# Kernel tuning notes

Hardware: AMD Instinct MI355X
Metric: run time of the kernel (lower is better)

The kernel has to match this reference:

```python
import jax, jax.numpy as jnp
import numpy as np

K = 3  # kernel size
PAD = 1
STRIDE = 1


def conv3x3(x, w, b):
    # x: [B,C,H,W], w: [O,I,3,3], b: [O]
    y = jax.lax.conv_general_dilated(
        x, w, window_strides=(STRIDE, STRIDE), padding=[(PAD, PAD), (PAD, PAD)],
        dimension_numbers=("NCHW", "OIHW", "NCHW"))
    return y + b[None, :, None, None]


def deform_conv2d(x, offsets, w, b):
    # x: [B,C,H,W]; offsets: [B,2*K*K,H,W] layout (dy,dx) per kernel tap;
    # w: [O,C,K,K]; b: [O]. stride=1, pad=1, dilation=1 (matches module).
    B, C, H, W = x.shape
    K2 = K * K
    off = offsets.reshape(B, K2, 2, H, W)
    dy, dx = off[:, :, 0], off[:, :, 1]  # [B,K2,H,W]

    ki, kj = jnp.meshgrid(jnp.arange(K), jnp.arange(K), indexing="ij")
    rel_y = (ki - PAD).reshape(K2).astype(x.dtype)  # kernel tap offsets
    rel_x = (kj - PAD).reshape(K2).astype(x.dtype)
    hh = jnp.arange(H, dtype=x.dtype)
    ww = jnp.arange(W, dtype=x.dtype)

    # sampling positions [B,K2,H,W]
    py = hh[None, None, :, None] + rel_y[None, :, None, None] + dy
    px = ww[None, None, None, :] + rel_x[None, :, None, None] + dx

    y0 = jnp.floor(py)
    x0 = jnp.floor(px)
    wy = py - y0  # bilinear weights
    wx = px - x0
    y0i = y0.astype(jnp.int32)
    x0i = x0.astype(jnp.int32)

    xf = x.reshape(B, C, H * W)

    def gather(yi, xi):
        valid = ((yi >= 0) & (yi < H) & (xi >= 0) & (xi < W)).astype(x.dtype)
        yc = jnp.clip(yi, 0, H - 1)
        xc = jnp.clip(xi, 0, W - 1)
        idx = (yc * W + xc).reshape(B, 1, K2 * H * W)
        v = jnp.take_along_axis(xf, idx, axis=2).reshape(B, C, K2, H, W)
        return v * valid.reshape(B, 1, K2, H, W)

    w00 = ((1 - wy) * (1 - wx))[:, None]  # [B,1,K2,H,W]
    w01 = ((1 - wy) * wx)[:, None]
    w10 = (wy * (1 - wx))[:, None]
    w11 = (wy * wx)[:, None]

    val = (w00 * gather(y0i, x0i) + w01 * gather(y0i, x0i + 1)
           + w10 * gather(y0i + 1, x0i) + w11 * gather(y0i + 1, x0i + 1))
    # accumulate over channels and kernel taps
    out = jnp.einsum("ock,bckhw->bohw", w.reshape(w.shape[0], C, K2), val)
    return out + b[None, :, None, None]


def setup_inputs() -> dict:
    key = jax.random.key(0)
    k1, k2, k3, k4 = jax.random.split(key, 4)
    B, Cin, Cout, H, W = 4, 256, 256, 80, 80
    x = jax.random.normal(k1, (B, Cin, H, W), dtype=jnp.float32)
    # offset-predicting conv: small init so predicted offsets are modest
    offset_w = jax.random.normal(k2, (2 * K * K, Cin, 3, 3), dtype=jnp.float32) * 0.01
    offset_b = jnp.zeros((2 * K * K,), dtype=jnp.float32)
    conv_w = jax.random.normal(k3, (Cout, Cin, K, K), dtype=jnp.float32) * (1.0 / np.sqrt(Cin * K * K))
    conv_b = jax.random.normal(k4, (Cout,), dtype=jnp.float32) * 0.01
    return {"x": x, "offset_w": offset_w, "offset_b": offset_b,
            "conv_w": conv_w, "conv_b": conv_b}


def reference(x, offset_w, offset_b, conv_w, conv_b):
    offsets = conv3x3(x, offset_w, offset_b)
    return deform_conv2d(x, offsets, conv_w, conv_b)
```

## Files before the change

### kernel.cpp

```cpp
#include <hip/hip_runtime.h>

#define CB 4
#define CIN 256
#define COUT 256
#define HH 80
#define WW 80
#define HW (HH*WW)
#define K2 9
#define NKC 72
#define LDSROW 56
#define NSTRIP (HW/64)
#define NBLK (CB*NSTRIP)

typedef unsigned short ushort_t;
typedef __attribute__((ext_vector_type(8))) short bf16x8;
typedef __attribute__((ext_vector_type(4))) float f32x4;

__device__ __forceinline__ ushort_t f2bf(float f) {
    unsigned int b = __float_as_uint(f);
    b += 0x7fffu + ((b >> 16) & 1u);
    return (ushort_t)(b >> 16);
}
__device__ __forceinline__ float bflo(unsigned int u) { return __uint_as_float(u << 16); }
__device__ __forceinline__ float bfhi(unsigned int u) { return __uint_as_float(u & 0xffff0000u); }

__device__ __forceinline__ unsigned int blendpack(unsigned int a, unsigned int b,
                                                  unsigned int c, unsigned int d,
                                                  float w0, float w1, float w2, float w3) {
    float lo = w0*bflo(a) + w1*bflo(b) + w2*bflo(c) + w3*bflo(d);
    float hi = w0*bfhi(a) + w1*bfhi(b) + w2*bfhi(c) + w3*bfhi(d);
    unsigned int r;
    asm("v_cvt_pk_bf16_f32 %0, %1, %2" : "=v"(r) : "v"(lo), "v"(hi));
    return r;
}

__global__ __launch_bounds__(256) void prep(const float* __restrict__ x,
                                            const float* __restrict__ conv_w,
                                            const float* __restrict__ offset_w,
                                            ushort_t* __restrict__ xb,
                                            ushort_t* __restrict__ wmain,
                                            ushort_t* __restrict__ woff) {
    __shared__ ushort_t tile[64*256];
    const int tid = threadIdx.x;
    if (blockIdx.x < NBLK) {
        const int b = blockIdx.x / NSTRIP;
        const int hw0 = (blockIdx.x % NSTRIP) * 64;
        const int px4 = (tid & 15) * 4;
        const int cb0 = tid >> 4;
        const float* xp = x + (size_t)b*CIN*HW + hw0 + px4;
        #pragma unroll
        for (int p = 0; p < 16; ++p) {
            const int c = cb0 * 16 + p;
            const float4 v = *(const float4*)(xp + (size_t)c*HW);
            const int blk = c >> 3, sub = c & 7;
            tile[(px4+0)*256 + (((blk) ^ ((px4+0)&31))<<3) + sub] = f2bf(v.x);
            tile[(px4+1)*256 + (((blk) ^ ((px4+1)&31))<<3) + sub] = f2bf(v.y);
            tile[(px4+2)*256 + (((blk) ^ ((px4+2)&31))<<3) + sub] = f2bf(v.z);
            tile[(px4+3)*256 + (((blk) ^ ((px4+3)&31))<<3) + sub] = f2bf(v.w);
        }
        __syncthreads();
        const int g = tid & 31;
        #pragma unroll
        for (int p = 0; p < 8; ++p) {
            const int px = (tid >> 5) + p*8;
            const uint4 r = *(const uint4*)&tile[px*256 + ((g ^ (px&31))<<3)];
            *(uint4*)&xb[((size_t)b*HW + hw0 + px)*CIN + g*8] = r;
        }
    } else {
        const int t = (blockIdx.x - NBLK) * 256 + tid;
        if (t < NKC*16*64) {
            const int kc = t >> 10;
            const int mt = (t >> 6) & 15;
            const int l  = t & 63;
            const int m  = mt*16 + (l & 15);
            const int kb = kc*32 + ((l >> 4) << 3);
            ushort_t v[8];
            #pragma unroll
            for (int i = 0; i < 8; ++i) {
                const int kg = kb + i;
                const int tap = kg >> 8;
                const int c = kg & 255;
                v[i] = f2bf(conv_w[(size_t)(m*CIN + c)*K2 + tap]);
            }
            uint4 r;
            r.x = v[0] | ((unsigned)v[1] << 16);
            r.y = v[2] | ((unsigned)v[3] << 16);
            r.z = v[4] | ((unsigned)v[5] << 16);
            r.w = v[6] | ((unsigned)v[7] << 16);
            *(uint4*)&wmain[(size_t)t*8] = r;
        } else if (t < NKC*16*64 + NKC*2*64) {
            const int t2 = t - NKC*16*64;
            const int kc = t2 >> 7;
            const int mt = (t2 >> 6) & 1;
            const int l  = t2 & 63;
            const int m  = mt*16 + (l & 15);
            const int kb = kc*32 + ((l >> 4) << 3);
            ushort_t v[8];
            #pragma unroll
            for (int i = 0; i < 8; ++i) {
                const int kg = kb + i;
                const int tap = kg >> 8;
                const int c = kg & 255;
                v[i] = (m < 18) ? f2bf(offset_w[(size_t)(m*CIN + c)*K2 + tap]) : (ushort_t)0;
            }
            uint4 r;
            r.x = v[0] | ((unsigned)v[1] << 16);
            r.y = v[2] | ((unsigned)v[3] << 16);
            r.z = v[4] | ((unsigned)v[5] << 16);
            r.w = v[6] | ((unsigned)v[7] << 16);
            *(uint4*)&woff[(size_t)t2*8] = r;
        }
    }
}

template<int BUF>
__device__ __forceinline__ void p3step(int kc, const ushort_t* __restrict__ xbase,
                                       const ushort_t* __restrict__ wmain,
                                       ushort_t* __restrict__ ldsB,
                                       const float (&bw)[K2][64][4], const int (&bi)[K2][64][4],
                                       uint4 &A0, uint4 &A1, uint4 &A2, uint4 &A3, float4 &wtA,
                                       bf16x8 (&afU)[4], bf16x8 (&afI)[4], f32x4 (&acc)[4][4],
                                       int pxg, int cg, int lane, int mt0) {
    float4 wtT; int4 ixT;
    const bool have = (kc + 2) < NKC;
    if (have) {
        const int tapT = (kc + 2) >> 3;
        wtT = *(const float4*)bw[tapT][pxg];
        ixT = *(const int4*)bi[tapT][pxg];
    }
    if (kc + 1 < NKC) {
        #pragma unroll
        for (int mi = 0; mi < 4; ++mi)
            afI[mi] = *(const bf16x8*)(wmain + ((size_t)((kc+1)*16 + mt0 + mi)*64 + lane)*8);
    }
    uint4 r;
    r.x = blendpack(A0.x, A1.x, A2.x, A3.x, wtA.x, wtA.y, wtA.z, wtA.w);
    r.y = blendpack(A0.y, A1.y, A2.y, A3.y, wtA.x, wtA.y, wtA.z, wtA.w);
    r.z = blendpack(A0.z, A1.z, A2.z, A3.z, wtA.x, wtA.y, wtA.z, wtA.w);
    r.w = blendpack(A0.w, A1.w, A2.w, A3.w, wtA.x, wtA.y, wtA.z, wtA.w);
    *(uint4*)&ldsB[BUF*64*LDSROW + pxg*LDSROW + cg*8] = r;
    if (have) {
        const int c0n = ((kc+2) & 7)*32 + cg*8;
        A0 = *(const uint4*)(xbase + ixT.x + c0n);
        A1 = *(const uint4*)(xbase + ixT.y + c0n);
        A2 = *(const uint4*)(xbase + ixT.z + c0n);
        A3 = *(const uint4*)(xbase + ixT.w + c0n);
        wtA = wtT;
    }
    asm volatile("s_waitcnt lgkmcnt(0)" ::: "memory");
    __builtin_amdgcn_s_barrier();
    bf16x8 bfr[4];
    #pragma unroll
    for (int ni = 0; ni < 4; ++ni)
        bfr[ni] = *(const bf16x8*)&ldsB[BUF*64*LDSROW + (ni*16 + (lane&15))*LDSROW + (lane>>4)*8];
    #pragma unroll
    for (int mi = 0; mi < 4; ++mi)
        #pragma unroll
        for (int ni = 0; ni < 4; ++ni)
            acc[mi][ni] = __builtin_amdgcn_mfma_f32_16x16x32_bf16(afU[mi], bfr[ni], acc[mi][ni], 0, 0, 0);
}

__global__ __launch_bounds__(256) void deform_main(const ushort_t* __restrict__ xb,
                                                   const ushort_t* __restrict__ wmain,
                                                   const ushort_t* __restrict__ woff,
                                                   const float* __restrict__ offset_b,
                                                   const float* __restrict__ conv_b,
                                                   float* __restrict__ out) {
    __shared__ __align__(16) char lds_pool[20480];
    __shared__ float off_lds[18][64];
    __shared__ float bw[K2][64][4];
    __shared__ int   bi[K2][64][4];

    const int tid = threadIdx.x;
    const int lane = tid & 63;
    const int wv = tid >> 6;
    const int sb = (blockIdx.x & 7) * (NBLK/8) + (blockIdx.x >> 3);
    const int bb = sb / NSTRIP;
    const int hwb = (sb % NSTRIP) * 64;
    const ushort_t* xbase = xb + (size_t)bb * HW * CIN;
    const int pxg = tid >> 2, cg = tid & 3;

    {
        const int mt = wv >> 1;
        const int p0 = (wv & 1) * 32;
        ushort_t* myB = (ushort_t*)lds_pool + wv * 2560;
        f32x4 a0 = {0.f,0.f,0.f,0.f}, a1 = {0.f,0.f,0.f,0.f};
        const int pxl = lane >> 1;
        const int ch  = lane & 1;
        const int hw = hwb + p0 + pxl;
        const int ph = hw / WW, pw = hw - ph*WW;

        uint4 u0a, u0b, u1a, u1b;
        #define P1LOAD(UA, UB, KC_) { \
            const int tap_ = (KC_) >> 3; \
            const int c0_ = ((KC_) & 7)*32 + ch*16; \
            const int yy_ = ph + tap_/3 - 1, xx_ = pw + tap_%3 - 1; \
            UA = make_uint4(0u,0u,0u,0u); UB = make_uint4(0u,0u,0u,0u); \
            if (yy_ >= 0 && yy_ < HH && xx_ >= 0 && xx_ < WW) { \
                const ushort_t* p_ = xbase + (yy_*WW + xx_)*CIN + c0_; \
                UA = *(const uint4*)p_; UB = *(const uint4*)(p_ + 8); } }

        P1LOAD(u0a, u0b, 0);
        P1LOAD(u1a, u1b, 1);
        for (int kp = 0; kp < NKC/2; ++kp) {
            {
                const int kc = 2*kp;
                const bf16x8 af = *(const bf16x8*)(woff + ((size_t)(kc*2 + mt)*64 + lane)*8);
                ushort_t* wb = myB + pxl*40 + ch*16;
                *(uint4*)wb = u0a;
                *(uint4*)(wb + 8) = u0b;
                if (kp + 1 < NKC/2) P1LOAD(u0a, u0b, 2*kp + 2);
                const bf16x8 b0 = *(const bf16x8*)(myB + (lane&15)*40 + (lane>>4)*8);
                const bf16x8 b1 = *(const bf16x8*)(myB + (16 + (lane&15))*40 + (lane>>4)*8);
                a0 = __builtin_amdgcn_mfma_f32_16x16x32_bf16(af, b0, a0, 0, 0, 0);
                a1 = __builtin_amdgcn_mfma_f32_16x16x32_bf16(af, b1, a1, 0, 0, 0);
            }
            {
                const int kc = 2*kp + 1;
                const bf16x8 af = *(const bf16x8*)(woff + ((size_t)(kc*2 + mt)*64 + lane)*8);
                ushort_t* wb = myB + 1280 + pxl*40 + ch*16;
                *(uint4*)wb = u1a;
                *(uint4*)(wb + 8) = u1b;
                if (kp + 1 < NKC/2) P1LOAD(u1a, u1b, 2*kp + 3);
                const bf16x8 b0 = *(const bf16x8*)(myB + 1280 + (lane&15)*40 + (lane>>4)*8);
                const bf16x8 b1 = *(const bf16x8*)(myB + 1280 + (16 + (lane&15))*40 + (lane>>4)*8);
                a0 = __builtin_amdgcn_mfma_f32_16x16x32_bf16(af, b0, a0, 0, 0, 0);
                a1 = __builtin_amdgcn_mfma_f32_16x16x32_bf16(af, b1, a1, 0, 0, 0);
            }
        }
        #undef P1LOAD
        const int r0 = (lane >> 4) * 4;
        #pragma unroll
        for (int j = 0; j < 4; ++j) {
            const int oc = mt*16 + r0 + j;
            if (oc < 18) {
                const float ob = offset_b[oc];
                off_lds[oc][p0 + (lane & 15)]      = a0[j] + ob;
                off_lds[oc][p0 + 16 + (lane & 15)] = a1[j] + ob;
            }
        }
    }
    __syncthreads();

    for (int it = tid; it < K2*64; it += 256) {
        const int tap = it >> 6, pxl = it & 63;
        const int hw = hwb + pxl;
        const int ph = hw / WW, pw = hw - ph*WW;
        const float dy = off_lds[tap*2][pxl];
        const float dx = off_lds[tap*2 + 1][pxl];
        const float py  = (float)(ph + tap/3 - 1) + dy;
        const float pxx = (float)(pw + tap%3 - 1) + dx;
        const float y0f = floorf(py), x0f = floorf(pxx);
        const float wy = py - y0f, wx = pxx - x0f;
        const int y0 = (int)y0f, x0 = (int)x0f;
        const int y1 = y0 + 1, x1 = x0 + 1;
        const float vy0 = (y0 >= 0 && y0 < HH) ? 1.f : 0.f;
        const float vy1 = (y1 >= 0 && y1 < HH) ? 1.f : 0.f;
        const float vx0 = (x0 >= 0 && x0 < WW) ? 1.f : 0.f;
        const float vx1 = (x1 >= 0 && x1 < WW) ? 1.f : 0.f;
        const int y0c = min(max(y0, 0), HH-1), y1c = min(max(y1, 0), HH-1);
        const int x0c = min(max(x0, 0), WW-1), x1c = min(max(x1, 0), WW-1);
        bw[tap][pxl][0] = (1.f-wy)*(1.f-wx)*vy0*vx0;
        bw[tap][pxl][1] = (1.f-wy)*wx*vy0*vx1;
        bw[tap][pxl][2] = wy*(1.f-wx)*vy1*vx0;
        bw[tap][pxl][3] = wy*wx*vy1*vx1;
        bi[tap][pxl][0] = (y0c*WW + x0c)*CIN;
        bi[tap][pxl][1] = (y0c*WW + x1c)*CIN;
        bi[tap][pxl][2] = (y1c*WW + x0c)*CIN;
        bi[tap][pxl][3] = (y1c*WW + x1c)*CIN;
    }
    __syncthreads();

    f32x4 acc[4][4];
    #pragma unroll
    for (int mi = 0; mi < 4; ++mi)
        #pragma unroll
        for (int ni = 0; ni < 4; ++ni)
            acc[mi][ni] = (f32x4){0.f,0.f,0.f,0.f};

    ushort_t* ldsB = (ushort_t*)lds_pool;
    const int mt0 = wv * 4;
    float4 wtA, wtB;
    uint4 A0, A1, A2, A3, B0, B1, B2, B3;
    bf16x8 afA[4], afB[4];
    {
        wtA = *(const float4*)bw[0][pxg];
        const int4 ix0 = *(const int4*)bi[0][pxg];
        const int c00 = cg*8;
        A0 = *(const uint4*)(xbase + ix0.x + c00);
        A1 = *(const uint4*)(xbase + ix0.y + c00);
        A2 = *(const uint4*)(xbase + ix0.z + c00);
        A3 = *(const uint4*)(xbase + ix0.w + c00);
        wtB = *(const float4*)bw[0][pxg];
        const int4 ix1 = *(const int4*)bi[0][pxg];
        const int c01 = 32 + cg*8;
        B0 = *(const uint4*)(xbase + ix1.x + c01);
        B1 = *(const uint4*)(xbase + ix1.y + c01);
        B2 = *(const uint4*)(xbase + ix1.z + c01);
        B3 = *(const uint4*)(xbase + ix1.w + c01);
        #pragma unroll
        for (int mi = 0; mi < 4; ++mi)
            afA[mi] = *(const bf16x8*)(wmain + ((size_t)(mt0 + mi)*64 + lane)*8);
    }
    for (int kp = 0; kp < NKC/2; ++kp) {
        p3step<0>(2*kp,     xbase, wmain, ldsB, bw, bi, A0, A1, A2, A3, wtA, afA, afB, acc, pxg, cg, lane, mt0);
        p3step<1>(2*kp + 1, xbase, wmain, ldsB, bw, bi, B0, B1, B2, B3, wtB, afB, afA, acc, pxg, cg, lane, mt0);
    }

    #pragma unroll
    for (int mi = 0; mi < 4; ++mi) {
        #pragma unroll
        for (int ni = 0; ni < 4; ++ni) {
            const int pxl = ni*16 + (lane & 15);
            #pragma unroll
            for (int j = 0; j < 4; ++j) {
                const int o = (mt0 + mi)*16 + (lane >> 4)*4 + j;
                out[((size_t)bb*COUT + o)*HW + hwb + pxl] = acc[mi][ni][j] + conv_b[o];
            }
        }
    }
}

extern "C" void kernel_launch(void* const* d_in, const int* in_sizes, int n_in,
                              void* d_out, int out_size, void* d_ws, size_t ws_size,
                              hipStream_t stream) {
    const float* x        = (const float*)d_in[0];
    const float* offset_w = (const float*)d_in[1];
    const float* offset_b = (const float*)d_in[2];
    const float* conv_w   = (const float*)d_in[3];
    const float* conv_b   = (const float*)d_in[4];
    float* out = (float*)d_out;

    char* wsb = (char*)d_ws;
    ushort_t* xb    = (ushort_t*)wsb;
    ushort_t* wmain = (ushort_t*)(wsb + (size_t)CB*HW*CIN*2);
    ushort_t* woff  = (ushort_t*)(wsb + (size_t)CB*HW*CIN*2 + (size_t)NKC*16*64*8*2);

    hipLaunchKernelGGL(prep, dim3(NBLK + 324), dim3(256), 0, stream,
                       x, conv_w, offset_w, xb, wmain, woff);
    hipLaunchKernelGGL(deform_main, dim3(NBLK), dim3(256), 0, stream,
                       xb, wmain, woff, offset_b, conv_b, out);
}
```

Before: 158.0 us.

## Halve pixel strip per block and restructure prep transpose and weight repack via LDS

The main kernel now handles 32 pixels per block instead of 64, which doubles the grid to 800 blocks and shrinks the accumulators, LDS buffers and per-thread gather width to match. The offset-conv phase is reshaped to one 16x16 tile per wave. The prep kernel now transposes x in 64-channel by 64-pixel tiles across 1600 blocks, and the weights are repacked by staging whole output-channel rows in LDS so global reads are coalesced. The aim is better CU occupancy and load balance on a 256-CU part and faster prep, at the cost of halving MFMA reuse of each A fragment and loading the weights twice as often.

```diff
diff --git a/kernel.cpp b/kernel.cpp
--- a/kernel.cpp
+++ b/kernel.cpp
@@ -8,9 +8,10 @@
 #define HW (HH*WW)
 #define K2 9
 #define NKC 72
-#define LDSROW 56
-#define NSTRIP (HW/64)
+#define PXB 32
+#define NSTRIP (HW/PXB)
 #define NBLK (CB*NSTRIP)
+#define LROW 40
 
 typedef unsigned short ushort_t;
 typedef __attribute__((ext_vector_type(8))) short bf16x8;
@@ -40,75 +41,72 @@
                                             ushort_t* __restrict__ xb,
                                             ushort_t* __restrict__ wmain,
                                             ushort_t* __restrict__ woff) {
-    __shared__ ushort_t tile[64*256];
     const int tid = threadIdx.x;
-    if (blockIdx.x < NBLK) {
-        const int b = blockIdx.x / NSTRIP;
-        const int hw0 = (blockIdx.x % NSTRIP) * 64;
+    if (blockIdx.x < 1600) {
+        __shared__ ushort_t tile[64*64];
+        const int b   = blockIdx.x / 400;
+        const int sub = blockIdx.x % 400;
+        const int hw0 = (sub % 100) * 64;
+        const int c0  = (sub / 100) * 64;
         const int px4 = (tid & 15) * 4;
-        const int cb0 = tid >> 4;
-        const float* xp = x + (size_t)b*CIN*HW + hw0 + px4;
-        #pragma unroll
-        for (int p = 0; p < 16; ++p) {
-            const int c = cb0 * 16 + p;
-            const float4 v = *(const float4*)(xp + (size_t)c*HW);
-            const int blk = c >> 3, sub = c & 7;
-            tile[(px4+0)*256 + (((blk) ^ ((px4+0)&31))<<3) + sub] = f2bf(v.x);
-            tile[(px4+1)*256 + (((blk) ^ ((px4+1)&31))<<3) + sub] = f2bf(v.y);
-            tile[(px4+2)*256 + (((blk) ^ ((px4+2)&31))<<3) + sub] = f2bf(v.z);
-            tile[(px4+3)*256 + (((blk) ^ ((px4+3)&31))<<3) + sub] = f2bf(v.w);
+        const int s   = tid & 7;
+        const float* xp = x + ((size_t)b*CIN + c0)*HW + hw0 + px4;
+        #pragma unroll
+        for (int p = 0; p < 4; ++p) {
+            const int cl = (tid >> 4) + p*16;
+            const float4 v = *(const float4*)(xp + (size_t)cl*HW);
+            const int cs = cl ^ (s << 3);
+            tile[(px4+0)*64 + cs] = f2bf(v.x);
+            tile[(px4+1)*64 + cs] = f2bf(v.y);
+            tile[(px4+2)*64 + cs] = f2bf(v.z);
+            tile[(px4+3)*64 + cs] = f2bf(v.w);
         }
         __syncthreads();
-        const int g = tid & 31;
-        #pragma unroll
-        for (int p = 0; p < 8; ++p) {
-            const int px = (tid >> 5) + p*8;
-            const uint4 r = *(const uint4*)&tile[px*256 + ((g ^ (px&31))<<3)];
-            *(uint4*)&xb[((size_t)b*HW + hw0 + px)*CIN + g*8] = r;
+        const int g = tid & 7;
+        #pragma unroll
+        for (int p = 0; p < 2; ++p) {
+            const int px = (tid >> 3) + p*32;
+            const int sr = (px >> 2) & 7;
+            const uint4 r = *(const uint4*)&tile[px*64 + ((g ^ sr) << 3)];
+            *(uint4*)&xb[((size_t)b*HW + hw0 + px)*CIN + c0 + g*8] = r;
         }
     } else {
-        const int t = (blockIdx.x - NBLK) * 256 + tid;
-        if (t < NKC*16*64) {
-            const int kc = t >> 10;
-            const int mt = (t >> 6) & 15;
-            const int l  = t & 63;
-            const int m  = mt*16 + (l & 15);
+        const bool isOff = (blockIdx.x >= 1616);
+        const int mt = isOff ? (int)(blockIdx.x - 1616) : (int)(blockIdx.x - 1600);
+        const float* src = isOff ? offset_w : conv_w;
+        ushort_t* dst = isOff ? woff : wmain;
+        __shared__ ushort_t wlds[16*2312];
+        const int mbase = mt*16;
+        for (int it = 0; it < 36; ++it) {
+            const int f4 = it*256 + tid;
+            const int ml = f4 / 576;
+            const int inner = (f4 - ml*576) * 4;
+            float4 v = make_float4(0.f,0.f,0.f,0.f);
+            if (!isOff || (mbase + ml) < 18)
+                v = *(const float4*)(src + ((size_t)(mbase + ml)*2304 + inner));
+            ushort_t* wp = &wlds[ml*2312 + inner];
+            wp[0] = f2bf(v.x); wp[1] = f2bf(v.y); wp[2] = f2bf(v.z); wp[3] = f2bf(v.w);
+        }
+        __syncthreads();
+        for (int it = 0; it < 18; ++it) {
+            const int e = it*256 + tid;
+            const int kc = e >> 6, l = e & 63;
+            const int ml = l & 15;
             const int kb = kc*32 + ((l >> 4) << 3);
             ushort_t v[8];
             #pragma unroll
             for (int i = 0; i < 8; ++i) {
                 const int kg = kb + i;
-                const int tap = kg >> 8;
-                const int c = kg & 255;
-                v[i] = f2bf(conv_w[(size_t)(m*CIN + c)*K2 + tap]);
+                v[i] = wlds[ml*2312 + (kg & 255)*9 + (kg >> 8)];
             }
             uint4 r;
             r.x = v[0] | ((unsigned)v[1] << 16);
             r.y = v[2] | ((unsigned)v[3] << 16);
             r.z = v[4] | ((unsigned)v[5] << 16);
             r.w = v[6] | ((unsigned)v[7] << 16);
-            *(uint4*)&wmain[(size_t)t*8] = r;
-        } else if (t < NKC*16*64 + NKC*2*64) {
-            const int t2 = t - NKC*16*64;
-            const int kc = t2 >> 7;
-            const int mt = (t2 >> 6) & 1;
-            const int l  = t2 & 63;
-            const int m  = mt*16 + (l & 15);
-            const int kb = kc*32 + ((l >> 4) << 3);
-            ushort_t v[8];
-            #pragma unroll
-            for (int i = 0; i < 8; ++i) {
-                const int kg = kb + i;
-                const int tap = kg >> 8;
-                const int c = kg & 255;
-                v[i] = (m < 18) ? f2bf(offset_w[(size_t)(m*CIN + c)*K2 + tap]) : (ushort_t)0;
-            }
-            uint4 r;
-            r.x = v[0] | ((unsigned)v[1] << 16);
-            r.y = v[2] | ((unsigned)v[3] << 16);
-            r.z = v[4] | ((unsigned)v[5] << 16);
-            r.w = v[6] | ((unsigned)v[7] << 16);
-            *(uint4*)&woff[(size_t)t2*8] = r;
+            const size_t o = isOff ? ((size_t)(kc*2 + mt)*64 + l)*8
+                                   : ((size_t)(kc*16 + mt)*64 + l)*8;
+            *(uint4*)&dst[o] = r;
         }
     }
 }
@@ -117,10 +115,10 @@
 __device__ __forceinline__ void p3step(int kc, const ushort_t* __restrict__ xbase,
                                        const ushort_t* __restrict__ wmain,
                                        ushort_t* __restrict__ ldsB,
-                                       const float (&bw)[K2][64][4], const int (&bi)[K2][64][4],
-                                       uint4 &A0, uint4 &A1, uint4 &A2, uint4 &A3, float4 &wtA,
-                                       bf16x8 (&afU)[4], bf16x8 (&afI)[4], f32x4 (&acc)[4][4],
-                                       int pxg, int cg, int lane, int mt0) {
+                                       const float (&bw)[K2][PXB][4], const int (&bi)[K2][PXB][4],
+                                       uint2 &A0, uint2 &A1, uint2 &A2, uint2 &A3, float4 &wtA,
+                                       bf16x8 (&afU)[4], bf16x8 (&afI)[4], f32x4 (&acc)[4][2],
+                                       int pxg, int cg8, int lane, int mt0) {
     float4 wtT; int4 ixT;
     const bool have = (kc + 2) < NKC;
     if (have) {
@@ -133,30 +131,28 @@
         for (int mi = 0; mi < 4; ++mi)
             afI[mi] = *(const bf16x8*)(wmain + ((size_t)((kc+1)*16 + mt0 + mi)*64 + lane)*8);
     }
-    uint4 r;
+    uint2 r;
     r.x = blendpack(A0.x, A1.x, A2.x, A3.x, wtA.x, wtA.y, wtA.z, wtA.w);
     r.y = blendpack(A0.y, A1.y, A2.y, A3.y, wtA.x, wtA.y, wtA.z, wtA.w);
-    r.z = blendpack(A0.z, A1.z, A2.z, A3.z, wtA.x, wtA.y, wtA.z, wtA.w);
-    r.w = blendpack(A0.w, A1.w, A2.w, A3.w, wtA.x, wtA.y, wtA.z, wtA.w);
-    *(uint4*)&ldsB[BUF*64*LDSROW + pxg*LDSROW + cg*8] = r;
+    *(uint2*)&ldsB[BUF*PXB*LROW + pxg*LROW + cg8*4] = r;
     if (have) {
-        const int c0n = ((kc+2) & 7)*32 + cg*8;
-        A0 = *(const uint4*)(xbase + ixT.x + c0n);
-        A1 = *(const uint4*)(xbase + ixT.y + c0n);
-        A2 = *(const uint4*)(xbase + ixT.z + c0n);
-        A3 = *(const uint4*)(xbase + ixT.w + c0n);
+        const int c0n = ((kc+2) & 7)*32 + cg8*4;
+        A0 = *(const uint2*)(xbase + ixT.x + c0n);
+        A1 = *(const uint2*)(xbase + ixT.y + c0n);
+        A2 = *(const uint2*)(xbase + ixT.z + c0n);
+        A3 = *(const uint2*)(xbase + ixT.w + c0n);
         wtA = wtT;
     }
     asm volatile("s_waitcnt lgkmcnt(0)" ::: "memory");
     __builtin_amdgcn_s_barrier();
-    bf16x8 bfr[4];
+    bf16x8 bfr[2];
     #pragma unroll
-    for (int ni = 0; ni < 4; ++ni)
-        bfr[ni] = *(const bf16x8*)&ldsB[BUF*64*LDSROW + (ni*16 + (lane&15))*LDSROW + (lane>>4)*8];
+    for (int ni = 0; ni < 2; ++ni)
+        bfr[ni] = *(const bf16x8*)&ldsB[BUF*PXB*LROW + (ni*16 + (lane&15))*LROW + (lane>>4)*8];
     #pragma unroll
     for (int mi = 0; mi < 4; ++mi)
         #pragma unroll
-        for (int ni = 0; ni < 4; ++ni)
+        for (int ni = 0; ni < 2; ++ni)
             acc[mi][ni] = __builtin_amdgcn_mfma_f32_16x16x32_bf16(afU[mi], bfr[ni], acc[mi][ni], 0, 0, 0);
 }
 
@@ -166,66 +162,56 @@
                                                    const float* __restrict__ offset_b,
                                                    const float* __restrict__ conv_b,
                                                    float* __restrict__ out) {
-    __shared__ __align__(16) char lds_pool[20480];
-    __shared__ float off_lds[18][64];
-    __shared__ float bw[K2][64][4];
-    __shared__ int   bi[K2][64][4];
+    __shared__ __align__(16) ushort_t lds_pool[4*2*16*LROW];
+    __shared__ float off_lds[18][PXB];
+    __shared__ float bw[K2][PXB][4];
+    __shared__ int   bi[K2][PXB][4];
 
     const int tid = threadIdx.x;
     const int lane = tid & 63;
     const int wv = tid >> 6;
     const int sb = (blockIdx.x & 7) * (NBLK/8) + (blockIdx.x >> 3);
     const int bb = sb / NSTRIP;
-    const int hwb = (sb % NSTRIP) * 64;
+    const int hwb = (sb % NSTRIP) * PXB;
     const ushort_t* xbase = xb + (size_t)bb * HW * CIN;
-    const int pxg = tid >> 2, cg = tid & 3;
 
     {
         const int mt = wv >> 1;
-        const int p0 = (wv & 1) * 32;
-        ushort_t* myB = (ushort_t*)lds_pool + wv * 2560;
-        f32x4 a0 = {0.f,0.f,0.f,0.f}, a1 = {0.f,0.f,0.f,0.f};
-        const int pxl = lane >> 1;
-        const int ch  = lane & 1;
-        const int hw = hwb + p0 + pxl;
+        const int nt = wv & 1;
+        ushort_t* myB = lds_pool + wv * (2*16*LROW);
+        f32x4 a0 = {0.f,0.f,0.f,0.f};
+        const int pxl = lane >> 2;
+        const int cgp = lane & 3;
+        const int hw = hwb + nt*16 + pxl;
         const int ph = hw / WW, pw = hw - ph*WW;
 
-        uint4 u0a, u0b, u1a, u1b;
-        #define P1LOAD(UA, UB, KC_) { \
+        uint4 u0, u1;
+        #define P1LOAD(U, KC_) { \
             const int tap_ = (KC_) >> 3; \
-            const int c0_ = ((KC_) & 7)*32 + ch*16; \
+            const int c0_ = ((KC_) & 7)*32 + cgp*8; \
             const int yy_ = ph + tap_/3 - 1, xx_ = pw + tap_%3 - 1; \
-            UA = make_uint4(0u,0u,0u,0u); UB = make_uint4(0u,0u,0u,0u); \
-            if (yy_ >= 0 && yy_ < HH && xx_ >= 0 && xx_ < WW) { \
-                const ushort_t* p_ = xbase + (yy_*WW + xx_)*CIN + c0_; \
-                UA = *(const uint4*)p_; UB = *(const uint4*)(p_ + 8); } }
-
-        P1LOAD(u0a, u0b, 0);
-        P1LOAD(u1a, u1b, 1);
+            U = make_uint4(0u,0u,0u,0u); \
+            if (yy_ >= 0 && yy_ < HH && xx_ >= 0 && xx_ < WW) \
+                U = *(const uint4*)(xbase + (yy_*WW + xx_)*CIN + c0_); }
+
+        P1LOAD(u0, 0);
+        P1LOAD(u1, 1);
         for (int kp = 0; kp < NKC/2; ++kp) {
             {
                 const int kc = 2*kp;
                 const bf16x8 af = *(const bf16x8*)(woff + ((size_t)(kc*2 + mt)*64 + lane)*8);
-                ushort_t* wb = myB + pxl*40 + ch*16;
-                *(uint4*)wb = u0a;
-                *(uint4*)(wb + 8) = u0b;
-                if (kp + 1 < NKC/2) P1LOAD(u0a, u0b, 2*kp + 2);
-                const bf16x8 b0 = *(const bf16x8*)(myB + (lane&15)*40 + (lane>>4)*8);
-                const bf16x8 b1 = *(const bf16x8*)(myB + (16 + (lane&15))*40 + (lane>>4)*8);
+                *(uint4*)&myB[pxl*LROW + cgp*8] = u0;
+                if (kp + 1 < NKC/2) P1LOAD(u0, 2*kp + 2);
+                const bf16x8 b0 = *(const bf16x8*)&myB[(lane&15)*LROW + (lane>>4)*8];
                 a0 = __builtin_amdgcn_mfma_f32_16x16x32_bf16(af, b0, a0, 0, 0, 0);
-                a1 = __builtin_amdgcn_mfma_f32_16x16x32_bf16(af, b1, a1, 0, 0, 0);
             }
             {
                 const int kc = 2*kp + 1;
                 const bf16x8 af = *(const bf16x8*)(woff + ((size_t)(kc*2 + mt)*64 + lane)*8);
-                ushort_t* wb = myB + 1280 + pxl*40 + ch*16;
-                *(uint4*)wb = u1a;
-                *(uint4*)(wb + 8) = u1b;
-                if (kp + 1 < NKC/2) P1LOAD(u1a, u1b, 2*kp + 3);
-                const bf16x8 b0 = *(const bf16x8*)(myB + 1280 + (lane&15)*40 + (lane>>4)*8);
-                const bf16x8 b1 = *(const bf16x8*)(myB + 1280 + (16 + (lane&15))*40 + (lane>>4)*8);
+                *(uint4*)&myB[16*LROW + pxl*LROW + cgp*8] = u1;
+                if (kp + 1 < NKC/2) P1LOAD(u1, 2*kp + 3);
+                const bf16x8 b0 = *(const bf16x8*)&myB[16*LROW + (lane&15)*LROW + (lane>>4)*8];
                 a0 = __builtin_amdgcn_mfma_f32_16x16x32_bf16(af, b0, a0, 0, 0, 0);
-                a1 = __builtin_amdgcn_mfma_f32_16x16x32_bf16(af, b1, a1, 0, 0, 0);
             }
         }
         #undef P1LOAD
@@ -233,17 +219,14 @@
         #pragma unroll
         for (int j = 0; j < 4; ++j) {
             const int oc = mt*16 + r0 + j;
-            if (oc < 18) {
-                const float ob = offset_b[oc];
-                off_lds[oc][p0 + (lane & 15)]      = a0[j] + ob;
-                off_lds[oc][p0 + 16 + (lane & 15)] = a1[j] + ob;
-            }
+            if (oc < 18)
+                off_lds[oc][nt*16 + (lane & 15)] = a0[j] + offset_b[oc];
         }
     }
     __syncthreads();
 
-    for (int it = tid; it < K2*64; it += 256) {
-        const int tap = it >> 6, pxl = it & 63;
+    for (int it = tid; it < K2*PXB; it += 256) {
+        const int tap = it >> 5, pxl = it & 31;
         const int hw = hwb + pxl;
         const int ph = hw / WW, pw = hw - ph*WW;
         const float dy = off_lds[tap*2][pxl];
@@ -271,46 +254,46 @@
     }
     __syncthreads();
 
-    f32x4 acc[4][4];
+    f32x4 acc[4][2];
     #pragma unroll
     for (int mi = 0; mi < 4; ++mi)
         #pragma unroll
-        for (int ni = 0; ni < 4; ++ni)
+        for (int ni = 0; ni < 2; ++ni)
             acc[mi][ni] = (f32x4){0.f,0.f,0.f,0.f};
 
-    ushort_t* ldsB = (ushort_t*)lds_pool;
+    ushort_t* ldsB = lds_pool;
     const int mt0 = wv * 4;
+    const int pxg = tid >> 3, cg8 = tid & 7;
     float4 wtA, wtB;
-    uint4 A0, A1, A2, A3, B0, B1, B2, B3;
+    uint2 A0, A1, A2, A3, B0, B1, B2, B3;
     bf16x8 afA[4], afB[4];
     {
         wtA = *(const float4*)bw[0][pxg];
         const int4 ix0 = *(const int4*)bi[0][pxg];
-        const int c00 = cg*8;
-        A0 = *(const uint4*)(xbase + ix0.x + c00);
-        A1 = *(const uint4*)(xbase + ix0.y + c00);
-        A2 = *(const uint4*)(xbase + ix0.z + c00);
-        A3 = *(const uint4*)(xbase + ix0.w + c00);
-        wtB = *(const float4*)bw[0][pxg];
-        const int4 ix1 = *(const int4*)bi[0][pxg];
-        const int c01 = 32 + cg*8;
-        B0 = *(const uint4*)(xbase + ix1.x + c01);
-        B1 = *(const uint4*)(xbase + ix1.y + c01);
-        B2 = *(const uint4*)(xbase + ix1.z + c01);
-        B3 = *(const uint4*)(xbase + ix1.w + c01);
+        const int c00 = cg8*4;
+        A0 = *(const uint2*)(xbase + ix0.x + c00);
+        A1 = *(const uint2*)(xbase + ix0.y + c00);
+        A2 = *(const uint2*)(xbase + ix0.z + c00);
+        A3 = *(const uint2*)(xbase + ix0.w + c00);
+        wtB = wtA;
+        const int c01 = 32 + cg8*4;
+        B0 = *(const uint2*)(xbase + ix0.x + c01);
+        B1 = *(const uint2*)(xbase + ix0.y + c01);
+        B2 = *(const uint2*)(xbase + ix0.z + c01);
+        B3 = *(const uint2*)(xbase + ix0.w + c01);
         #pragma unroll
         for (int mi = 0; mi < 4; ++mi)
             afA[mi] = *(const bf16x8*)(wmain + ((size_t)(mt0 + mi)*64 + lane)*8);
     }
     for (int kp = 0; kp < NKC/2; ++kp) {
-        p3step<0>(2*kp,     xbase, wmain, ldsB, bw, bi, A0, A1, A2, A3, wtA, afA, afB, acc, pxg, cg, lane, mt0);
-        p3step<1>(2*kp + 1, xbase, wmain, ldsB, bw, bi, B0, B1, B2, B3, wtB, afB, afA, acc, pxg, cg, lane, mt0);
+        p3step<0>(2*kp,     xbase, wmain, ldsB, bw, bi, A0, A1, A2, A3, wtA, afA, afB, acc, pxg, cg8, lane, mt0);
+        p3step<1>(2*kp + 1, xbase, wmain, ldsB, bw, bi, B0, B1, B2, B3, wtB, afB, afA, acc, pxg, cg8, lane, mt0);
     }
 
     #pragma unroll
     for (int mi = 0; mi < 4; ++mi) {
         #pragma unroll
-        for (int ni = 0; ni < 4; ++ni) {
+        for (int ni = 0; ni < 2; ++ni) {
             const int pxl = ni*16 + (lane & 15);
             #pragma unroll
             for (int j = 0; j < 4; ++j) {
@@ -336,7 +319,7 @@
     ushort_t* wmain = (ushort_t*)(wsb + (size_t)CB*HW*CIN*2);
     ushort_t* woff  = (ushort_t*)(wsb + (size_t)CB*HW*CIN*2 + (size_t)NKC*16*64*8*2);
 
-    hipLaunchKernelGGL(prep, dim3(NBLK + 324), dim3(256), 0, stream,
+    hipLaunchKernelGGL(prep, dim3(1618), dim3(256), 0, stream,
                        x, conv_w, offset_w, xb, wmain, woff);
     hipLaunchKernelGGL(deform_main, dim3(NBLK), dim3(256), 0, stream,
                        xb, wmain, woff, offset_b, conv_b, out);
```

Measured after the change: 205.4 us. +30.0%, slower.

## Switch to fp16 with packed half2 bilinear blending and restructure prep kernel

Applied to the files above, without the earlier changes.

Converts activations and weights to fp16 instead of bf16 and uses fp16 MFMA. The bilinear blend becomes packed half2 multiply-adds with pre-packed half2 weights, replacing the per-element fp32 unpack, FMA and repack. The prep kernel is restructured: the x transpose uses smaller 64x64 tiles across more blocks, and the weight reorder stages rows in LDS so global reads are coalesced instead of strided. Accumulating the blend in fp16 and the narrower fp16 range add rounding and overflow risk relative to bf16 with fp32 blending.

```diff
diff --git a/kernel.cpp b/kernel.cpp
--- a/kernel.cpp
+++ b/kernel.cpp
@@ -13,25 +13,23 @@
 #define NBLK (CB*NSTRIP)
 
 typedef unsigned short ushort_t;
-typedef __attribute__((ext_vector_type(8))) short bf16x8;
+typedef __attribute__((ext_vector_type(8))) _Float16 f16x8;
+typedef __attribute__((ext_vector_type(2))) _Float16 h2;
 typedef __attribute__((ext_vector_type(4))) float f32x4;
 
-__device__ __forceinline__ ushort_t f2bf(float f) {
-    unsigned int b = __float_as_uint(f);
-    b += 0x7fffu + ((b >> 16) & 1u);
-    return (ushort_t)(b >> 16);
-}
-__device__ __forceinline__ float bflo(unsigned int u) { return __uint_as_float(u << 16); }
-__device__ __forceinline__ float bfhi(unsigned int u) { return __uint_as_float(u & 0xffff0000u); }
-
-__device__ __forceinline__ unsigned int blendpack(unsigned int a, unsigned int b,
-                                                  unsigned int c, unsigned int d,
-                                                  float w0, float w1, float w2, float w3) {
-    float lo = w0*bflo(a) + w1*bflo(b) + w2*bflo(c) + w3*bflo(d);
-    float hi = w0*bfhi(a) + w1*bfhi(b) + w2*bfhi(c) + w3*bfhi(d);
-    unsigned int r;
-    asm("v_cvt_pk_bf16_f32 %0, %1, %2" : "=v"(r) : "v"(lo), "v"(hi));
-    return r;
+__device__ __forceinline__ ushort_t f2h(float f) {
+    _Float16 h = (_Float16)f;
+    return *(ushort_t*)&h;
+}
+
+__device__ __forceinline__ unsigned int blend2(unsigned int a, unsigned int b,
+                                               unsigned int c, unsigned int d,
+                                               h2 w0, h2 w1, h2 w2, h2 w3) {
+    h2 r = *(h2*)&a * w0;
+    r += *(h2*)&b * w1;
+    r += *(h2*)&c * w2;
+    r += *(h2*)&d * w3;
+    return *(unsigned int*)&r;
 }
 
 __global__ __launch_bounds__(256) void prep(const float* __restrict__ x,
@@ -40,75 +38,72 @@
                                             ushort_t* __restrict__ xb,
                                             ushort_t* __restrict__ wmain,
                                             ushort_t* __restrict__ woff) {
-    __shared__ ushort_t tile[64*256];
     const int tid = threadIdx.x;
-    if (blockIdx.x < NBLK) {
-        const int b = blockIdx.x / NSTRIP;
-        const int hw0 = (blockIdx.x % NSTRIP) * 64;
+    if (blockIdx.x < 1600) {
+        __shared__ ushort_t tile[64*64];
+        const int b   = blockIdx.x / 400;
+        const int sub = blockIdx.x % 400;
+        const int hw0 = (sub % 100) * 64;
+        const int c0  = (sub / 100) * 64;
         const int px4 = (tid & 15) * 4;
-        const int cb0 = tid >> 4;
-        const float* xp = x + (size_t)b*CIN*HW + hw0 + px4;
-        #pragma unroll
-        for (int p = 0; p < 16; ++p) {
-            const int c = cb0 * 16 + p;
-            const float4 v = *(const float4*)(xp + (size_t)c*HW);
-            const int blk = c >> 3, sub = c & 7;
-            tile[(px4+0)*256 + (((blk) ^ ((px4+0)&31))<<3) + sub] = f2bf(v.x);
-            tile[(px4+1)*256 + (((blk) ^ ((px4+1)&31))<<3) + sub] = f2bf(v.y);
-            tile[(px4+2)*256 + (((blk) ^ ((px4+2)&31))<<3) + sub] = f2bf(v.z);
-            tile[(px4+3)*256 + (((blk) ^ ((px4+3)&31))<<3) + sub] = f2bf(v.w);
+        const int s   = tid & 7;
+        const float* xp = x + ((size_t)b*CIN + c0)*HW + hw0 + px4;
+        #pragma unroll
+        for (int p = 0; p < 4; ++p) {
+            const int cl = (tid >> 4) + p*16;
+            const float4 v = *(const float4*)(xp + (size_t)cl*HW);
+            const int cs = cl ^ (s << 3);
+            tile[(px4+0)*64 + cs] = f2h(v.x);
+            tile[(px4+1)*64 + cs] = f2h(v.y);
+            tile[(px4+2)*64 + cs] = f2h(v.z);
+            tile[(px4+3)*64 + cs] = f2h(v.w);
         }
         __syncthreads();
-        const int g = tid & 31;
-        #pragma unroll
-        for (int p = 0; p < 8; ++p) {
-            const int px = (tid >> 5) + p*8;
-            const uint4 r = *(const uint4*)&tile[px*256 + ((g ^ (px&31))<<3)];
-            *(uint4*)&xb[((size_t)b*HW + hw0 + px)*CIN + g*8] = r;
+        const int g = tid & 7;
+        #pragma unroll
+        for (int p = 0; p < 2; ++p) {
+            const int px = (tid >> 3) + p*32;
+            const int sr = (px >> 2) & 7;
+            const uint4 r = *(const uint4*)&tile[px*64 + ((g ^ sr) << 3)];
+            *(uint4*)&xb[((size_t)b*HW + hw0 + px)*CIN + c0 + g*8] = r;
         }
     } else {
-        const int t = (blockIdx.x - NBLK) * 256 + tid;
-        if (t < NKC*16*64) {
-            const int kc = t >> 10;
-            const int mt = (t >> 6) & 15;
-            const int l  = t & 63;
-            const int m  = mt*16 + (l & 15);
+        const bool isOff = (blockIdx.x >= 1616);
+        const int mt = isOff ? (int)(blockIdx.x - 1616) : (int)(blockIdx.x - 1600);
+        const float* src = isOff ? offset_w : conv_w;
+        ushort_t* dst = isOff ? woff : wmain;
+        __shared__ ushort_t wlds[16*2312];
+        const int mbase = mt*16;
+        for (int it = 0; it < 36; ++it) {
+            const int f4 = it*256 + tid;
+            const int ml = f4 / 576;
+            const int inner = (f4 - ml*576) * 4;
+            float4 v = make_float4(0.f,0.f,0.f,0.f);
+            if (!isOff || (mbase + ml) < 18)
+                v = *(const float4*)(src + ((size_t)(mbase + ml)*2304 + inner));
+            ushort_t* wp = &wlds[ml*2312 + inner];
+            wp[0] = f2h(v.x); wp[1] = f2h(v.y); wp[2] = f2h(v.z); wp[3] = f2h(v.w);
+        }
+        __syncthreads();
+        for (int it = 0; it < 18; ++it) {
+            const int e = it*256 + tid;
+            const int kc = e >> 6, l = e & 63;
+            const int ml = l & 15;
             const int kb = kc*32 + ((l >> 4) << 3);
             ushort_t v[8];
             #pragma unroll
             for (int i = 0; i < 8; ++i) {
                 const int kg = kb + i;
-                const int tap = kg >> 8;
-                const int c = kg & 255;
-                v[i] = f2bf(conv_w[(size_t)(m*CIN + c)*K2 + tap]);
+                v[i] = wlds[ml*2312 + (kg & 255)*9 + (kg >> 8)];
             }
             uint4 r;
             r.x = v[0] | ((unsigned)v[1] << 16);
             r.y = v[2] | ((unsigned)v[3] << 16);
             r.z = v[4] | ((unsigned)v[5] << 16);
             r.w = v[6] | ((unsigned)v[7] << 16);
-            *(uint4*)&wmain[(size_t)t*8] = r;
-        } else if (t < NKC*16*64 + NKC*2*64) {
-            const int t2 = t - NKC*16*64;
-            const int kc = t2 >> 7;
-            const int mt = (t2 >> 6) & 1;
-            const int l  = t2 & 63;
-            const int m  = mt*16 + (l & 15);
-            const int kb = kc*32 + ((l >> 4) << 3);
-            ushort_t v[8];
-            #pragma unroll
-            for (int i = 0; i < 8; ++i) {
-                const int kg = kb + i;
-                const int tap = kg >> 8;
-                const int c = kg & 255;
-                v[i] = (m < 18) ? f2bf(offset_w[(size_t)(m*CIN + c)*K2 + tap]) : (ushort_t)0;
-            }
-            uint4 r;
-            r.x = v[0] | ((unsigned)v[1] << 16);
-            r.y = v[2] | ((unsigned)v[3] << 16);
-            r.z = v[4] | ((unsigned)v[5] << 16);
-            r.w = v[6] | ((unsigned)v[7] << 16);
-            *(uint4*)&woff[(size_t)t2*8] = r;
+            const size_t o = isOff ? ((size_t)(kc*2 + mt)*64 + l)*8
+                                   : ((size_t)(kc*16 + mt)*64 + l)*8;
+            *(uint4*)&dst[o] = r;
         }
     }
 }
@@ -117,28 +112,31 @@
 __device__ __forceinline__ void p3step(int kc, const ushort_t* __restrict__ xbase,
                                        const ushort_t* __restrict__ wmain,
                                        ushort_t* __restrict__ ldsB,
-                                       const float (&bw)[K2][64][4], const int (&bi)[K2][64][4],
-                                       uint4 &A0, uint4 &A1, uint4 &A2, uint4 &A3, float4 &wtA,
-                                       bf16x8 (&afU)[4], bf16x8 (&afI)[4], f32x4 (&acc)[4][4],
+                                       const uint4 (&bwp)[K2][64], const int4 (&bip)[K2][64],
+                                       uint4 &A0, uint4 &A1, uint4 &A2, uint4 &A3, uint4 &wtA,
+                                       f16x8 (&afU)[4], f16x8 (&afI)[4], f32x4 (&acc)[4][4],
                                        int pxg, int cg, int lane, int mt0) {
-    float4 wtT; int4 ixT;
+    uint4 wtT; int4 ixT;
     const bool have = (kc + 2) < NKC;
     if (have) {
         const int tapT = (kc + 2) >> 3;
-        wtT = *(const float4*)bw[tapT][pxg];
-        ixT = *(const int4*)bi[tapT][pxg];
+        wtT = bwp[tapT][pxg];
+        ixT = bip[tapT][pxg];
     }
     if (kc + 1 < NKC) {
         #pragma unroll
         for (int mi = 0; mi < 4; ++mi)
-            afI[mi] = *(const bf16x8*)(wmain + ((size_t)((kc+1)*16 + mt0 + mi)*64 + lane)*8);
-    }
-    uint4 r;
-    r.x = blendpack(A0.x, A1.x, A2.x, A3.x, wtA.x, wtA.y, wtA.z, wtA.w);
-    r.y = blendpack(A0.y, A1.y, A2.y, A3.y, wtA.x, wtA.y, wtA.z, wtA.w);
-    r.z = blendpack(A0.z, A1.z, A2.z, A3.z, wtA.x, wtA.y, wtA.z, wtA.w);
-    r.w = blendpack(A0.w, A1.w, A2.w, A3.w, wtA.x, wtA.y, wtA.z, wtA.w);
-    *(uint4*)&ldsB[BUF*64*LDSROW + pxg*LDSROW + cg*8] = r;
+            afI[mi] = *(const f16x8*)(wmain + ((size_t)((kc+1)*16 + mt0 + mi)*64 + lane)*8);
+    }
+    {
+        const h2 w0 = *(h2*)&wtA.x, w1 = *(h2*)&wtA.y, w2 = *(h2*)&wtA.z, w3 = *(h2*)&wtA.w;
+        uint4 r;
+        r.x = blend2(A0.x, A1.x, A2.x, A3.x, w0, w1, w2, w3);
+        r.y = blend2(A0.y, A1.y, A2.y, A3.y, w0, w1, w2, w3);
+        r.z = blend2(A0.z, A1.z, A2.z, A3.z, w0, w1, w2, w3);
+        r.w = blend2(A0.w, A1.w, A2.w, A3.w, w0, w1, w2, w3);
+        *(uint4*)&ldsB[BUF*64*LDSROW + pxg*LDSROW + cg*8] = r;
+    }
     if (have) {
         const int c0n = ((kc+2) & 7)*32 + cg*8;
         A0 = *(const uint4*)(xbase + ixT.x + c0n);
@@ -149,15 +147,15 @@
     }
     asm volatile("s_waitcnt lgkmcnt(0)" ::: "memory");
     __builtin_amdgcn_s_barrier();
-    bf16x8 bfr[4];
+    f16x8 bfr[4];
     #pragma unroll
     for (int ni = 0; ni < 4; ++ni)
-        bfr[ni] = *(const bf16x8*)&ldsB[BUF*64*LDSROW + (ni*16 + (lane&15))*LDSROW + (lane>>4)*8];
+        bfr[ni] = *(const f16x8*)&ldsB[BUF*64*LDSROW + (ni*16 + (lane&15))*LDSROW + (lane>>4)*8];
     #pragma unroll
     for (int mi = 0; mi < 4; ++mi)
         #pragma unroll
         for (int ni = 0; ni < 4; ++ni)
-            acc[mi][ni] = __builtin_amdgcn_mfma_f32_16x16x32_bf16(afU[mi], bfr[ni], acc[mi][ni], 0, 0, 0);
+            acc[mi][ni] = __builtin_amdgcn_mfma_f32_16x16x32_f16(afU[mi], bfr[ni], acc[mi][ni], 0, 0, 0);
 }
 
 __global__ __launch_bounds__(256) void deform_main(const ushort_t* __restrict__ xb,
@@ -168,8 +166,8 @@
                                                    float* __restrict__ out) {
     __shared__ __align__(16) char lds_pool[20480];
     __shared__ float off_lds[18][64];
-    __shared__ float bw[K2][64][4];
-    __shared__ int   bi[K2][64][4];
+    __shared__ uint4 bwp[K2][64];
+    __shared__ int4  bip[K2][64];
 
     const int tid = threadIdx.x;
     const int lane = tid & 63;
@@ -205,27 +203,27 @@
         for (int kp = 0; kp < NKC/2; ++kp) {
             {
                 const int kc = 2*kp;
-                const bf16x8 af = *(const bf16x8*)(woff + ((size_t)(kc*2 + mt)*64 + lane)*8);
+                const f16x8 af = *(const f16x8*)(woff + ((size_t)(kc*2 + mt)*64 + lane)*8);
                 ushort_t* wb = myB + pxl*40 + ch*16;
                 *(uint4*)wb = u0a;
                 *(uint4*)(wb + 8) = u0b;
                 if (kp + 1 < NKC/2) P1LOAD(u0a, u0b, 2*kp + 2);
-                const bf16x8 b0 = *(const bf16x8*)(myB + (lane&15)*40 + (lane>>4)*8);
-                const bf16x8 b1 = *(const bf16x8*)(myB + (16 + (lane&15))*40 + (lane>>4)*8);
-                a0 = __builtin_amdgcn_mfma_f32_16x16x32_bf16(af, b0, a0, 0, 0, 0);
-                a1 = __builtin_amdgcn_mfma_f32_16x16x32_bf16(af, b1, a1, 0, 0, 0);
+                const f16x8 b0 = *(const f16x8*)(myB + (lane&15)*40 + (lane>>4)*8);
+                const f16x8 b1 = *(const f16x8*)(myB + (16 + (lane&15))*40 + (lane>>4)*8);
+                a0 = __builtin_amdgcn_mfma_f32_16x16x32_f16(af, b0, a0, 0, 0, 0);
+                a1 = __builtin_amdgcn_mfma_f32_16x16x32_f16(af, b1, a1, 0, 0, 0);
             }
             {
                 const int kc = 2*kp + 1;
-                const bf16x8 af = *(const bf16x8*)(woff + ((size_t)(kc*2 + mt)*64 + lane)*8);
+                const f16x8 af = *(const f16x8*)(woff + ((size_t)(kc*2 + mt)*64 + lane)*8);
                 ushort_t* wb = myB + 1280 + pxl*40 + ch*16;
                 *(uint4*)wb = u1a;
                 *(uint4*)(wb + 8) = u1b;
                 if (kp + 1 < NKC/2) P1LOAD(u1a, u1b, 2*kp + 3);
-                const bf16x8 b0 = *(const bf16x8*)(myB + 1280 + (lane&15)*40 + (lane>>4)*8);
-                const bf16x8 b1 = *(const bf16x8*)(myB + 1280 + (16 + (lane&15))*40 + (lane>>4)*8);
-                a0 = __builtin_amdgcn_mfma_f32_16x16x32_bf16(af, b0, a0, 0, 0, 0);
-                a1 = __builtin_amdgcn_mfma_f32_16x16x32_bf16(af, b1, a1, 0, 0, 0);
+                const f16x8 b0 = *(const f16x8*)(myB + 1280 + (lane&15)*40 + (lane>>4)*8);
+                const f16x8 b1 = *(const f16x8*)(myB + 1280 + (16 + (lane&15))*40 + (lane>>4)*8);
+                a0 = __builtin_amdgcn_mfma_f32_16x16x32_f16(af, b0, a0, 0, 0, 0);
+                a1 = __builtin_amdgcn_mfma_f32_16x16x32_f16(af, b1, a1, 0, 0, 0);
             }
         }
         #undef P1LOAD
@@ -260,14 +258,18 @@
         const float vx1 = (x1 >= 0 && x1 < WW) ? 1.f : 0.f;
         const int y0c = min(max(y0, 0), HH-1), y1c = min(max(y1, 0), HH-1);
         const int x0c = min(max(x0, 0), WW-1), x1c = min(max(x1, 0), WW-1);
-        bw[tap][pxl][0] = (1.f-wy)*(1.f-wx)*vy0*vx0;
-        bw[tap][pxl][1] = (1.f-wy)*wx*vy0*vx1;
-        bw[tap][pxl][2] = wy*(1.f-wx)*vy1*vx0;
-        bw[tap][pxl][3] = wy*wx*vy1*vx1;
-        bi[tap][pxl][0] = (y0c*WW + x0c)*CIN;
-        bi[tap][pxl][1] = (y0c*WW + x1c)*CIN;
-        bi[tap][pxl][2] = (y1c*WW + x0c)*CIN;
-        bi[tap][pxl][3] = (y1c*WW + x1c)*CIN;
+        const float W00 = (1.f-wy)*(1.f-wx)*vy0*vx0;
+        const float W01 = (1.f-wy)*wx*vy0*vx1;
+        const float W10 = wy*(1.f-wx)*vy1*vx0;
+        const float W11 = wy*wx*vy1*vx1;
+        uint4 wv4;
+        { h2 t = {(_Float16)W00, (_Float16)W00}; wv4.x = *(unsigned int*)&t; }
+        { h2 t = {(_Float16)W01, (_Float16)W01}; wv4.y = *(unsigned int*)&t; }
+        { h2 t = {(_Float16)W10, (_Float16)W10}; wv4.z = *(unsigned int*)&t; }
+        { h2 t = {(_Float16)W11, (_Float16)W11}; wv4.w = *(unsigned int*)&t; }
+        bwp[tap][pxl] = wv4;
+        bip[tap][pxl] = make_int4((y0c*WW + x0c)*CIN, (y0c*WW + x1c)*CIN,
+                                  (y1c*WW + x0c)*CIN, (y1c*WW + x1c)*CIN);
     }
     __syncthreads();
 
@@ -280,31 +282,30 @@
 
     ushort_t* ldsB = (ushort_t*)lds_pool;
     const int mt0 = wv * 4;
-    float4 wtA, wtB;
+    uint4 wtA, wtB;
     uint4 A0, A1, A2, A3, B0, B1, B2, B3;
-    bf16x8 afA[4], afB[4];
+    f16x8 afA[4], afB[4];
     {
-        wtA = *(const float4*)bw[0][pxg];
-        const int4 ix0 = *(const int4*)bi[0][pxg];
+        wtA = bwp[0][pxg];
+        const int4 ix0 = bip[0][pxg];
         const int c00 = cg*8;
         A0 = *(const uint4*)(xbase + ix0.x + c00);
         A1 = *(const uint4*)(xbase + ix0.y + c00);
         A2 = *(const uint4*)(xbase + ix0.z + c00);
         A3 = *(const uint4*)(xbase + ix0.w + c00);
-        wtB = *(const float4*)bw[0][pxg];
-        const int4 ix1 = *(const int4*)bi[0][pxg];
+        wtB = wtA;
         const int c01 = 32 + cg*8;
-        B0 = *(const uint4*)(xbase + ix1.x + c01);
-        B1 = *(const uint4*)(xbase + ix1.y + c01);
-        B2 = *(const uint4*)(xbase + ix1.z + c01);
-        B3 = *(const uint4*)(xbase + ix1.w + c01);
+        B0 = *(const uint4*)(xbase + ix0.x + c01);
+        B1 = *(const uint4*)(xbase + ix0.y + c01);
+        B2 = *(const uint4*)(xbase + ix0.z + c01);
+        B3 = *(const uint4*)(xbase + ix0.w + c01);
         #pragma unroll
         for (int mi = 0; mi < 4; ++mi)
-            afA[mi] = *(const bf16x8*)(wmain + ((size_t)(mt0 + mi)*64 + lane)*8);
+            afA[mi] = *(const f16x8*)(wmain + ((size_t)(mt0 + mi)*64 + lane)*8);
     }
     for (int kp = 0; kp < NKC/2; ++kp) {
-        p3step<0>(2*kp,     xbase, wmain, ldsB, bw, bi, A0, A1, A2, A3, wtA, afA, afB, acc, pxg, cg, lane, mt0);
-        p3step<1>(2*kp + 1, xbase, wmain, ldsB, bw, bi, B0, B1, B2, B3, wtB, afB, afA, acc, pxg, cg, lane, mt0);
+        p3step<0>(2*kp,     xbase, wmain, ldsB, bwp, bip, A0, A1, A2, A3, wtA, afA, afB, acc, pxg, cg, lane, mt0);
+        p3step<1>(2*kp + 1, xbase, wmain, ldsB, bwp, bip, B0, B1, B2, B3, wtB, afB, afA, acc, pxg, cg, lane, mt0);
     }
 
     #pragma unroll
@@ -336,7 +337,7 @@
     ushort_t* wmain = (ushort_t*)(wsb + (size_t)CB*HW*CIN*2);
     ushort_t* woff  = (ushort_t*)(wsb + (size_t)CB*HW*CIN*2 + (size_t)NKC*16*64*8*2);
 
-    hipLaunchKernelGGL(prep, dim3(NBLK + 324), dim3(256), 0, stream,
+    hipLaunchKernelGGL(prep, dim3(1618), dim3(256), 0, stream,
                        x, conv_w, offset_w, xb, wmain, woff);
     hipLaunchKernelGGL(deform_main, dim3(NBLK), dim3(256), 0, stream,
                        xb, wmain, woff, offset_b, conv_b, out);
```

Result: slower. 181.8 us (+15.1%).
